# Kernel tuning notes

Hardware: AMD Instinct MI355X
Metric: run time of the kernel (lower is better)

The kernel has to match this reference:

```python
import jax, jax.numpy as jnp
import numpy as np

NCH, P, T, BS = 129, 4, 64000, 8
FRM_RATE, TC, HAIR_TC, SHFT, FAC = 16, 8.0, 0.5, 0, 1.0
L_FRM = FRM_RATE * (2 ** (4 + SHFT))            # 256 samples per frame
ALPHA = float(np.exp(-1.0 / (TC * 2 ** (4 + SHFT))))       # temporal integrator pole
BETA = float(np.exp(-1.0 / (HAIR_TC * 2 ** (4 + SHFT))))   # hair-cell LPF pole


def setup_inputs() -> dict:
    rng = np.random.default_rng(0)
    # stable order-4 cochlear IIRs: 2 conjugate pole pairs inside unit circle
    r = rng.uniform(0.8, 0.97, (NCH, P // 2))
    th = rng.uniform(0.05, np.pi - 0.05, (NCH, P // 2))
    A = np.stack([
        np.poly(np.concatenate([r[c] * np.exp(1j * th[c]), r[c] * np.exp(-1j * th[c])])).real
        for c in range(NCH)
    ]).astype(np.float32)                        # [NCH, P+1], A[:,0]==1
    B = (rng.standard_normal((NCH, P + 1)) * 0.1).astype(np.float32)
    key = jax.random.key(0)
    wav = jax.random.normal(key, (BS, T), dtype=jnp.float32)
    return {"wavData": wav, "coch_B": jnp.asarray(B), "coch_A": jnp.asarray(A)}


def iir_lfilter(b, a, x):
    # b, a: [nCh, P+1] (a[:,0] == 1), x: [bs, T] -> y: [nCh, bs, T]
    # direct-form II transposed, all channels in one scan over time
    bt = b[:, None, :]                           # [nCh, 1, P+1]
    at = a[:, None, :]
    z0 = jnp.zeros((b.shape[0], x.shape[0], b.shape[1] - 1), x.dtype)

    def step(z, xt):                             # z: [nCh, bs, P], xt: [bs]
        y = bt[..., 0] * xt[None, :] + z[..., 0]
        z_shift = jnp.concatenate([z[..., 1:], jnp.zeros_like(z[..., :1])], -1)
        z = z_shift + bt[..., 1:] * xt[None, :, None] - at[..., 1:] * y[..., None]
        return z, y

    _, y = jax.lax.scan(step, z0, x.T)           # y: [T, nCh, bs]
    return jnp.moveaxis(y, 0, -1)                # [nCh, bs, T]


def first_order_iir(x, c):
    # y[t] = x[t] + c * y[t-1] along the last axis (lfilter b=[1,0], a=[1,-c])
    def combine(e1, e2):
        a1, b1 = e1
        a2, b2 = e2
        return a1 * a2, b1 * a2 + b2

    coef = jnp.full_like(x, jnp.asarray(c, x.dtype))
    _, y = jax.lax.associative_scan(combine, (coef, x), axis=-1)
    return y


def reference(wavData, coch_B, coch_A):
    y1 = iir_lfilter(coch_B, coch_A, wavData)        # cochlear filterbank [nCh, bs, T]
    y2 = jax.nn.sigmoid(FAC * y1)                    # hair-cell nonlinearity
    y2 = first_order_iir(y2, BETA)                   # hair-cell membrane LPF
    y2_prev = jnp.concatenate([y2[:1], y2[:-1]], 0)  # previous channel (ch 0 diffs itself -> 0)
    y4 = jnp.maximum(y2 - y2_prev, 0.0)              # lateral inhibition + half-wave rectify
    y5 = first_order_iir(y4, ALPHA)                  # temporal integration (alpha != 0 branch)
    aud = y5[..., 0:T - 1:L_FRM]                     # frame-rate downsample [nCh, bs, nFrm]
    return jnp.transpose(aud, (1, 0, 2))             # [bs, nCh, nFrm]
```

## Files before the change

kernel.cpp:

```cpp
#include <hip/hip_runtime.h>
#include <math.h>

#define NCH 129
#define BS 8
#define TLEN 64000
#define TILE 256
#define WARM 64
#define NFRM 250
#define NSEQ (NCH * BS)
#define NBK (BS * NFRM)
#define KF_EDGE 8
#define KF_MAIN (NBK / 4)
#define GI 32
#define GW 16
#define GMAIN 64
#define MAXSEG 112

typedef float f2 __attribute__((ext_vector_type(2)));

__device__ __forceinline__ f2 mk2(float a, float b) { f2 r; r.x = a; r.y = b; return r; }

__device__ __forceinline__ f2 fma2(f2 a, f2 b, f2 c) {
#if __has_builtin(__builtin_elementwise_fma)
    return __builtin_elementwise_fma(a, b, c);
#else
    f2 r; r.x = fmaf(a.x, b.x, c.x); r.y = fmaf(a.y, b.y, c.y); return r;
#endif
}

__device__ __forceinline__ float sigf(float v) {
    return __builtin_amdgcn_rcpf(1.0f + __expf(-v));
}
__device__ __forceinline__ f2 sig2(f2 v) {
    f2 r; r.x = sigf(v.x); r.y = sigf(v.y); return r;
}

struct C2 { f2 b0, b1, b2, b3, b4, a1, a2, a3, a4; };

__device__ __forceinline__ C2 load_coef2(const float* __restrict__ B,
                                         const float* __restrict__ A,
                                         int cx, int cy) {
    C2 q;
    q.b0 = mk2(B[cx * 5 + 0], B[cy * 5 + 0]);
    q.b1 = mk2(B[cx * 5 + 1], B[cy * 5 + 1]);
    q.b2 = mk2(B[cx * 5 + 2], B[cy * 5 + 2]);
    q.b3 = mk2(B[cx * 5 + 3], B[cy * 5 + 3]);
    q.b4 = mk2(B[cx * 5 + 4], B[cy * 5 + 4]);
    q.a1 = mk2(A[cx * 5 + 1], A[cy * 5 + 1]);
    q.a2 = mk2(A[cx * 5 + 2], A[cy * 5 + 2]);
    q.a3 = mk2(A[cx * 5 + 3], A[cy * 5 + 3]);
    q.a4 = mk2(A[cx * 5 + 4], A[cy * 5 + 4]);
    return q;
}

__device__ __forceinline__ f2 iir2_step(const C2& q, float x,
                                        f2& z0, f2& z1, f2& z2, f2& z3) {
    f2 xx = mk2(x, x);
    f2 y = fma2(q.b0, xx, z0);
    z0 = fma2(-q.a1, y, fma2(q.b1, xx, z1));
    z1 = fma2(-q.a2, y, fma2(q.b2, xx, z2));
    z2 = fma2(-q.a3, y, fma2(q.b3, xx, z3));
    z3 = fma2(-q.a4, y, q.b4 * xx);
    return y;
}

#define ISTEP(xv) { (void)iir2_step(q, (xv), z0, z1, z2, z3); }
#define WSTEP(xv)                                                              \
    { f2 y_ = iir2_step(q, (xv), z0, z1, z2, z3);                              \
      u = fma2(beta2, u, sig2(y_)); }
#define MSTEP(xv)                                                              \
    { f2 y_ = iir2_step(q, (xv), z0, z1, z2, z3);                              \
      u = fma2(beta2, u, sig2(y_));                                            \
      float un_ = __shfl_down(u.x, 1, 64);                                     \
      float y4o_ = fmaxf(u.y - u.x, 0.0f);                                     \
      float y4e_ = fmaxf(pend_un - pend_ub, 0.0f);                             \
      g2 = fma2(alpha2, g2, mk2(y4o_, y4e_));                                  \
      pend_un = un_; pend_ub = u.y; }

__global__ __launch_bounds__(256, 8) void kF_fused(
        const float* __restrict__ wav, const float* __restrict__ B,
        const float* __restrict__ A, float* __restrict__ G,
        float* __restrict__ y4f, float beta, float alpha) {
    __shared__ float4 xs4[4 * MAXSEG];
    int blk = blockIdx.x;
    const f2 beta2 = mk2(beta, beta);
    const f2 alpha2 = mk2(alpha, alpha);

    if (blk < KF_EDGE) {
        int item = blk * 256 + threadIdx.x;
        if (item >= NBK) return;
        int b = item / NFRM;
        int r = item - b * NFRM;
        C2 q = load_coef2(B, A, 127, 128);
        f2 z0 = mk2(0.f, 0.f), z1 = z0, z2 = z0, z3 = z0, u = z0;
        int nIst = (r == 0) ? 0 : 4 * GI;
        int nW   = (r == 0) ? 0 : 4 * GW;
        const float* xg = wav + (size_t)b * TLEN
                        + (size_t)r * TILE - (size_t)(nIst + nW);
        #pragma unroll 2
        for (int j = 0; j < nIst; ++j) ISTEP(xg[j]);
        xg += nIst;
        #pragma unroll 2
        for (int j = 0; j < nW; ++j) WSTEP(xg[j]);
        xg += nW;
        float g4 = 0.f, yfirst = 0.f;
        #pragma unroll 2
        for (int j = 0; j < TILE; ++j) {
            f2 y_ = iir2_step(q, xg[j], z0, z1, z2, z3);
            u = fma2(beta2, u, sig2(y_));
            float y4 = fmaxf(u.y - u.x, 0.0f);
            if (j == 0) yfirst = y4;
            g4 = fmaf(alpha, g4, y4);
        }
        size_t idx = ((size_t)b * NFRM + r) * NCH + 128;
        G[idx] = g4;
        y4f[idx] = yfirst;
        return;
    }

    int wave = threadIdx.x >> 6;
    int t = threadIdx.x & 63;
    int tile = (blk - KF_EDGE) * 4 + wave;
    int b = tile / NFRM;
    int r = tile - b * NFRM;
    int gi = (r == 0) ? 0 : GI;
    int gw = (r == 0) ? 0 : GW;
    int gbase = gi + gw;
    int n4 = gbase + GMAIN;
    const float* xg = wav + (size_t)b * TLEN
                    + (size_t)r * TILE - (size_t)(4 * gbase);
    float4* seg = xs4 + wave * MAXSEG;
    for (int i = t; i < n4; i += 64) seg[i] = ((const float4*)xg)[i];
    __syncthreads();

    int cA = 2 * t, cB = 2 * t + 1;
    C2 q = load_coef2(B, A, cA, cB);
    f2 z0 = mk2(0.f, 0.f), z1 = z0, z2 = z0, z3 = z0, u = z0;
    for (int g = 0; g < gi; ++g) {
        float4 xq = seg[g];
        ISTEP(xq.x); ISTEP(xq.y); ISTEP(xq.z); ISTEP(xq.w);
    }
    for (int g = gi; g < gbase; ++g) {
        float4 xq = seg[g];
        WSTEP(xq.x); WSTEP(xq.y); WSTEP(xq.z); WSTEP(xq.w);
    }

    f2 g2;
    float fo, fe, pend_un, pend_ub;
    {
        float4 xq = seg[gbase];
        f2 y_ = iir2_step(q, xq.x, z0, z1, z2, z3);
        u = fma2(beta2, u, sig2(y_));
        float un_ = __shfl_down(u.x, 1, 64);
        float y4o_ = fmaxf(u.y - u.x, 0.0f);
        fo = y4o_;
        g2 = mk2(y4o_, 0.0f);
        pend_un = un_; pend_ub = u.y;
        y_ = iir2_step(q, xq.y, z0, z1, z2, z3);
        u = fma2(beta2, u, sig2(y_));
        un_ = __shfl_down(u.x, 1, 64);
        y4o_ = fmaxf(u.y - u.x, 0.0f);
        float y4e_ = fmaxf(pend_un - pend_ub, 0.0f);
        fe = y4e_;
        g2 = fma2(alpha2, g2, mk2(y4o_, y4e_));
        pend_un = un_; pend_ub = u.y;
        MSTEP(xq.z); MSTEP(xq.w);
    }
    for (int g = gbase + 1; g < gbase + GMAIN; ++g) {
        float4 xq = seg[g];
        MSTEP(xq.x); MSTEP(xq.y); MSTEP(xq.z); MSTEP(xq.w);
    }
    float y4e_last = fmaxf(pend_un - pend_ub, 0.0f);
    float go = g2.x;
    float ge = fmaf(alpha, g2.y, y4e_last);

    size_t base = ((size_t)b * NFRM + r) * NCH;
    G[base + cB] = go;
    y4f[base + cB] = fo;
    if (t < 63) {
        G[base + cB + 1] = ge;
        y4f[base + cB + 1] = fe;
    }
}

#define KD_LOAD(gn, yn, i)                                                     \
    {   int kk = k0 + (i); int kcl = (kk < NFRM) ? kk : (NFRM - 1);            \
        size_t ix = ((size_t)b * NFRM + kcl) * NCH + c;                        \
        gn = G[ix]; yn = y4f[ix];                                              \
        if (kk >= NFRM) { gn = 0.f; yn = 0.f; } }
#define KD_REPLAY(gn, yn, i)                                                   \
    {   int kk = k0 + (i);                                                     \
        if (kk < NFRM) o[kk] = fmaf(alpha, sv, yn);                            \
        sv = fmaf(aL, sv, gn); }

__global__ __launch_bounds__(256) void kD_scan_par(
        const float* __restrict__ G, const float* __restrict__ y4f,
        float* __restrict__ out, float alpha, float aL) {
    int id = blockIdx.x * 4 + (threadIdx.x >> 6);
    int lane = threadIdx.x & 63;
    if (id >= NSEQ) return;
    int b = id / NCH;
    int c = id - b * NCH;
    float* o = out + (size_t)id * NFRM;
    int k0 = lane * 4;
    if (c == 0) {
        #pragma unroll
        for (int i = 0; i < 4; ++i) {
            int kk = k0 + i;
            if (kk < NFRM) o[kk] = 0.0f;
        }
        return;
    }
    float g0, g1, g2v, g3, y0, y1, y2v, y3;
    KD_LOAD(g0, y0, 0); KD_LOAD(g1, y1, 1); KD_LOAD(g2v, y2v, 2); KD_LOAD(g3, y3, 3);
    float e = g0;
    e = fmaf(aL, e, g1);
    e = fmaf(aL, e, g2v);
    e = fmaf(aL, e, g3);
    float aL2 = aL * aL;
    float f = aL2 * aL2;
    for (int s = 0; s < 6; ++s) {
        int off = 1 << s;
        float src = __shfl_up(e, off, 64);
        if (lane < off) src = 0.f;
        e = fmaf(f, src, e);
        f = f * f;
    }
    float sv = __shfl_up(e, 1, 64);
    if (lane == 0) sv = 0.f;
    KD_REPLAY(g0, y0, 0); KD_REPLAY(g1, y1, 1);
    KD_REPLAY(g2v, y2v, 2); KD_REPLAY(g3, y3, 3);
}

extern "C" void kernel_launch(void* const* d_in, const int* in_sizes, int n_in,
                              void* d_out, int out_size, void* d_ws, size_t ws_size,
                              hipStream_t stream) {
    const float* wav = (const float*)d_in[0];
    const float* Bc  = (const float*)d_in[1];
    const float* Ac  = (const float*)d_in[2];
    float* out = (float*)d_out;

    float* G   = (float*)d_ws;
    float* y4f = G + (size_t)NBK * NCH;

    const float alpha  = (float)exp(-1.0 / 128.0);
    const float beta   = (float)exp(-1.0 / 8.0);
    const float alphaL = (float)exp(-256.0 / 128.0);

    kF_fused<<<KF_EDGE + KF_MAIN, 256, 0, stream>>>(wav, Bc, Ac, G, y4f, beta, alpha);
    kD_scan_par<<<NSEQ / 4, 256, 0, stream>>>(G, y4f, out, alpha, alphaL);
}
```

Baseline: 110.1 us.

## Interleave two independent batch IIR chains per thread to expose ILP

```diff
diff --git a/kernel.cpp b/kernel.cpp
--- a/kernel.cpp
+++ b/kernel.cpp
@@ -9,8 +9,8 @@
 #define NFRM 250
 #define NSEQ (NCH * BS)
 #define NBK (BS * NFRM)
-#define KF_EDGE 8
-#define KF_MAIN (NBK / 4)
+#define KF_EDGE 16
+#define KF_MAIN 500
 #define GI 32
 #define GW 16
 #define GMAIN 64
@@ -64,20 +64,21 @@
     return y;
 }
 
-#define ISTEP(xv) { (void)iir2_step(q, (xv), z0, z1, z2, z3); }
-#define WSTEP(xv)                                                              \
-    { f2 y_ = iir2_step(q, (xv), z0, z1, z2, z3);                              \
-      u = fma2(beta2, u, sig2(y_)); }
-#define MSTEP(xv)                                                              \
-    { f2 y_ = iir2_step(q, (xv), z0, z1, z2, z3);                              \
-      u = fma2(beta2, u, sig2(y_));                                            \
-      float un_ = __shfl_down(u.x, 1, 64);                                     \
-      float y4o_ = fmaxf(u.y - u.x, 0.0f);                                     \
-      float y4e_ = fmaxf(pend_un - pend_ub, 0.0f);                             \
-      g2 = fma2(alpha2, g2, mk2(y4o_, y4e_));                                  \
-      pend_un = un_; pend_ub = u.y; }
-
-__global__ __launch_bounds__(256, 8) void kF_fused(
+#define ISTEPX(xv, Z0, Z1, Z2, Z3)                                             \
+    { (void)iir2_step(q, (xv), Z0, Z1, Z2, Z3); }
+#define WSTEPX(xv, Z0, Z1, Z2, Z3, U)                                          \
+    { f2 y_ = iir2_step(q, (xv), Z0, Z1, Z2, Z3);                              \
+      U = fma2(beta2, U, sig2(y_)); }
+#define MSTEPX(xv, Z0, Z1, Z2, Z3, U, G2, PU, PB)                              \
+    { f2 y_ = iir2_step(q, (xv), Z0, Z1, Z2, Z3);                              \
+      U = fma2(beta2, U, sig2(y_));                                            \
+      float un_ = __shfl_down(U.x, 1, 64);                                     \
+      float y4o_ = fmaxf(U.y - U.x, 0.0f);                                     \
+      float y4e_ = fmaxf(PU - PB, 0.0f);                                       \
+      G2 = fma2(alpha2, G2, mk2(y4o_, y4e_));                                  \
+      PU = un_; PB = U.y; }
+
+__global__ __launch_bounds__(128, 4) void kF_fused(
         const float* __restrict__ wav, const float* __restrict__ B,
         const float* __restrict__ A, float* __restrict__ G,
         float* __restrict__ y4f, float beta, float alpha) {
@@ -87,7 +88,7 @@
     const f2 alpha2 = mk2(alpha, alpha);
 
     if (blk < KF_EDGE) {
-        int item = blk * 256 + threadIdx.x;
+        int item = blk * 128 + threadIdx.x;
         if (item >= NBK) return;
         int b = item / NFRM;
         int r = item - b * NFRM;
@@ -98,10 +99,10 @@
         const float* xg = wav + (size_t)b * TLEN
                         + (size_t)r * TILE - (size_t)(nIst + nW);
         #pragma unroll 2
-        for (int j = 0; j < nIst; ++j) ISTEP(xg[j]);
+        for (int j = 0; j < nIst; ++j) ISTEPX(xg[j], z0, z1, z2, z3);
         xg += nIst;
         #pragma unroll 2
-        for (int j = 0; j < nW; ++j) WSTEP(xg[j]);
+        for (int j = 0; j < nW; ++j) WSTEPX(xg[j], z0, z1, z2, z3, u);
         xg += nW;
         float g4 = 0.f, yfirst = 0.f;
         #pragma unroll 2
@@ -120,66 +121,104 @@
 
     int wave = threadIdx.x >> 6;
     int t = threadIdx.x & 63;
-    int tile = (blk - KF_EDGE) * 4 + wave;
-    int b = tile / NFRM;
-    int r = tile - b * NFRM;
+    int wid = (blk - KF_EDGE) * 2 + wave;
+    int bA = wid / NFRM;
+    int r  = wid - bA * NFRM;
+    int bB = bA + 4;
     int gi = (r == 0) ? 0 : GI;
     int gw = (r == 0) ? 0 : GW;
     int gbase = gi + gw;
     int n4 = gbase + GMAIN;
-    const float* xg = wav + (size_t)b * TLEN
-                    + (size_t)r * TILE - (size_t)(4 * gbase);
-    float4* seg = xs4 + wave * MAXSEG;
-    for (int i = t; i < n4; i += 64) seg[i] = ((const float4*)xg)[i];
+    size_t off = (size_t)r * TILE - (size_t)(4 * gbase);
+    const float* xgA = wav + (size_t)bA * TLEN + off;
+    const float* xgB = wav + (size_t)bB * TLEN + off;
+    float4* segA = xs4 + (wave * 2) * MAXSEG;
+    float4* segB = segA + MAXSEG;
+    for (int i = t; i < n4; i += 64) {
+        segA[i] = ((const float4*)xgA)[i];
+        segB[i] = ((const float4*)xgB)[i];
+    }
     __syncthreads();
 
     int cA = 2 * t, cB = 2 * t + 1;
     C2 q = load_coef2(B, A, cA, cB);
-    f2 z0 = mk2(0.f, 0.f), z1 = z0, z2 = z0, z3 = z0, u = z0;
+    f2 zA0 = mk2(0.f, 0.f), zA1 = zA0, zA2 = zA0, zA3 = zA0, uA = zA0;
+    f2 zB0 = zA0, zB1 = zA0, zB2 = zA0, zB3 = zA0, uB = zA0;
     for (int g = 0; g < gi; ++g) {
-        float4 xq = seg[g];
-        ISTEP(xq.x); ISTEP(xq.y); ISTEP(xq.z); ISTEP(xq.w);
+        float4 xa = segA[g], xb = segB[g];
+        ISTEPX(xa.x, zA0, zA1, zA2, zA3); ISTEPX(xb.x, zB0, zB1, zB2, zB3);
+        ISTEPX(xa.y, zA0, zA1, zA2, zA3); ISTEPX(xb.y, zB0, zB1, zB2, zB3);
+        ISTEPX(xa.z, zA0, zA1, zA2, zA3); ISTEPX(xb.z, zB0, zB1, zB2, zB3);
+        ISTEPX(xa.w, zA0, zA1, zA2, zA3); ISTEPX(xb.w, zB0, zB1, zB2, zB3);
     }
     for (int g = gi; g < gbase; ++g) {
-        float4 xq = seg[g];
-        WSTEP(xq.x); WSTEP(xq.y); WSTEP(xq.z); WSTEP(xq.w);
-    }
-
-    f2 g2;
-    float fo, fe, pend_un, pend_ub;
+        float4 xa = segA[g], xb = segB[g];
+        WSTEPX(xa.x, zA0, zA1, zA2, zA3, uA); WSTEPX(xb.x, zB0, zB1, zB2, zB3, uB);
+        WSTEPX(xa.y, zA0, zA1, zA2, zA3, uA); WSTEPX(xb.y, zB0, zB1, zB2, zB3, uB);
+        WSTEPX(xa.z, zA0, zA1, zA2, zA3, uA); WSTEPX(xb.z, zB0, zB1, zB2, zB3, uB);
+        WSTEPX(xa.w, zA0, zA1, zA2, zA3, uA); WSTEPX(xb.w, zB0, zB1, zB2, zB3, uB);
+    }
+
+    f2 g2A, g2B;
+    float foA, feA, puA, pbA, foB, feB, puB, pbB;
     {
-        float4 xq = seg[gbase];
-        f2 y_ = iir2_step(q, xq.x, z0, z1, z2, z3);
-        u = fma2(beta2, u, sig2(y_));
-        float un_ = __shfl_down(u.x, 1, 64);
-        float y4o_ = fmaxf(u.y - u.x, 0.0f);
-        fo = y4o_;
-        g2 = mk2(y4o_, 0.0f);
-        pend_un = un_; pend_ub = u.y;
-        y_ = iir2_step(q, xq.y, z0, z1, z2, z3);
-        u = fma2(beta2, u, sig2(y_));
-        un_ = __shfl_down(u.x, 1, 64);
-        y4o_ = fmaxf(u.y - u.x, 0.0f);
-        float y4e_ = fmaxf(pend_un - pend_ub, 0.0f);
-        fe = y4e_;
-        g2 = fma2(alpha2, g2, mk2(y4o_, y4e_));
-        pend_un = un_; pend_ub = u.y;
-        MSTEP(xq.z); MSTEP(xq.w);
+        float4 xa = segA[gbase], xb = segB[gbase];
+        f2 y_ = iir2_step(q, xa.x, zA0, zA1, zA2, zA3);
+        uA = fma2(beta2, uA, sig2(y_));
+        puA = __shfl_down(uA.x, 1, 64);
+        foA = fmaxf(uA.y - uA.x, 0.0f);
+        g2A = mk2(foA, 0.0f);
+        pbA = uA.y;
+        y_ = iir2_step(q, xb.x, zB0, zB1, zB2, zB3);
+        uB = fma2(beta2, uB, sig2(y_));
+        puB = __shfl_down(uB.x, 1, 64);
+        foB = fmaxf(uB.y - uB.x, 0.0f);
+        g2B = mk2(foB, 0.0f);
+        pbB = uB.y;
+        y_ = iir2_step(q, xa.y, zA0, zA1, zA2, zA3);
+        uA = fma2(beta2, uA, sig2(y_));
+        float un_ = __shfl_down(uA.x, 1, 64);
+        float y4o_ = fmaxf(uA.y - uA.x, 0.0f);
+        feA = fmaxf(puA - pbA, 0.0f);
+        g2A = fma2(alpha2, g2A, mk2(y4o_, feA));
+        puA = un_; pbA = uA.y;
+        y_ = iir2_step(q, xb.y, zB0, zB1, zB2, zB3);
+        uB = fma2(beta2, uB, sig2(y_));
+        un_ = __shfl_down(uB.x, 1, 64);
+        y4o_ = fmaxf(uB.y - uB.x, 0.0f);
+        feB = fmaxf(puB - pbB, 0.0f);
+        g2B = fma2(alpha2, g2B, mk2(y4o_, feB));
+        puB = un_; pbB = uB.y;
+        MSTEPX(xa.z, zA0, zA1, zA2, zA3, uA, g2A, puA, pbA);
+        MSTEPX(xb.z, zB0, zB1, zB2, zB3, uB, g2B, puB, pbB);
+        MSTEPX(xa.w, zA0, zA1, zA2, zA3, uA, g2A, puA, pbA);
+        MSTEPX(xb.w, zB0, zB1, zB2, zB3, uB, g2B, puB, pbB);
     }
     for (int g = gbase + 1; g < gbase + GMAIN; ++g) {
-        float4 xq = seg[g];
-        MSTEP(xq.x); MSTEP(xq.y); MSTEP(xq.z); MSTEP(xq.w);
-    }
-    float y4e_last = fmaxf(pend_un - pend_ub, 0.0f);
-    float go = g2.x;
-    float ge = fmaf(alpha, g2.y, y4e_last);
-
-    size_t base = ((size_t)b * NFRM + r) * NCH;
-    G[base + cB] = go;
-    y4f[base + cB] = fo;
+        float4 xa = segA[g], xb = segB[g];
+        MSTEPX(xa.x, zA0, zA1, zA2, zA3, uA, g2A, puA, pbA);
+        MSTEPX(xb.x, zB0, zB1, zB2, zB3, uB, g2B, puB, pbB);
+        MSTEPX(xa.y, zA0, zA1, zA2, zA3, uA, g2A, puA, pbA);
+        MSTEPX(xb.y, zB0, zB1, zB2, zB3, uB, g2B, puB, pbB);
+        MSTEPX(xa.z, zA0, zA1, zA2, zA3, uA, g2A, puA, pbA);
+        MSTEPX(xb.z, zB0, zB1, zB2, zB3, uB, g2B, puB, pbB);
+        MSTEPX(xa.w, zA0, zA1, zA2, zA3, uA, g2A, puA, pbA);
+        MSTEPX(xb.w, zB0, zB1, zB2, zB3, uB, g2B, puB, pbB);
+    }
+    float goA = g2A.x, geA = fmaf(alpha, g2A.y, fmaxf(puA - pbA, 0.0f));
+    float goB = g2B.x, geB = fmaf(alpha, g2B.y, fmaxf(puB - pbB, 0.0f));
+
+    size_t baseA = ((size_t)bA * NFRM + r) * NCH;
+    size_t baseB = ((size_t)bB * NFRM + r) * NCH;
+    G[baseA + cB] = goA;
+    y4f[baseA + cB] = foA;
+    G[baseB + cB] = goB;
+    y4f[baseB + cB] = foB;
     if (t < 63) {
-        G[base + cB + 1] = ge;
-        y4f[base + cB + 1] = fe;
+        G[baseA + cB + 1] = geA;
+        y4f[baseA + cB + 1] = feA;
+        G[baseB + cB + 1] = geB;
+        y4f[baseB + cB + 1] = feB;
     }
 }
 
@@ -247,6 +286,6 @@
     const float beta   = (float)exp(-1.0 / 8.0);
     const float alphaL = (float)exp(-256.0 / 128.0);
 
-    kF_fused<<<KF_EDGE + KF_MAIN, 256, 0, stream>>>(wav, Bc, Ac, G, y4f, beta, alpha);
+    kF_fused<<<KF_EDGE + KF_MAIN, 128, 0, stream>>>(wav, Bc, Ac, G, y4f, beta, alpha);
     kD_scan_par<<<NSEQ / 4, 256, 0, stream>>>(G, y4f, out, alpha, alphaL);
 }
```

Result: slower. 139.5 us (+26.7%).
